# Optimization experiments

Hardware: AMD Instinct MI355X
Metric: run time of the kernel (lower is better)

Reference implementation:

```python
import jax, jax.numpy as jnp
import numpy as np


def _sum_matrix():
    # [69, 42] mask matrix reproducing compute_sums exactly (incl. bugs):
    # feature k = sum over cells where M[k] == 1, board flattened row-major (6x7).
    M = np.zeros((69, 42), dtype=np.float32)
    m = M.reshape(69, 6, 7)
    # 24 row window sums
    for row in range(6):
        for i in range(4):
            m[row * 4 + i, row, i:i + 4] = 1.0
    # 21 column window sums
    for col in range(7):
        for i in range(3):
            m[24 + col * 3 + i, i:i + 4, col] = 1.0
    # 12 'upward diag' sums: source sums the FULL 4x4 block of the row-flipped
    # board, i.e. original rows (2-off)..(5-off), cols col..col+3.
    for off in range(3):
        for col in range(4):
            m[45 + off * 4 + col, 2 - off:6 - off, col:col + 4] = 1.0
    # 12 'downward diag' sums: allocated but never written in source -> zeros.
    return jnp.asarray(M)


_M = _sum_matrix()  # [69, 42]


def setup_inputs() -> dict:
    key = jax.random.key(0)
    k1, k2, k3 = jax.random.split(key, 3)
    B = 524288
    game_state = jax.random.normal(k1, (B, 42), dtype=jnp.float32)
    W = jax.random.normal(k2, (7, 111), dtype=jnp.float32) * (1.0 / np.sqrt(111.0))
    b = jax.random.normal(k3, (7,), dtype=jnp.float32) * 0.01
    return {"game_state": game_state, "W": W, "b": b}


def reference(game_state, W, b):
    # sums: [B, 69] = all windowed sums as one GEMM against the mask matrix
    sums = game_state @ _M.T
    feats = jnp.concatenate([game_state, sums], axis=1)  # [B, 111]
    return feats @ W.T + b  # [B, 7]
```

## Files before the change

kernel.cpp:

```cpp
#include <hip/hip_runtime.h>


#define TILE_ROWS 128
#define ROW_PAD   43

__global__ __launch_bounds__(320)
void ddqn_weff(const float* __restrict__ W, float* __restrict__ weff) {
    int tid = threadIdx.x;
    if (tid >= 7 * 42) return;
    int j = tid / 42;
    int d = tid % 42;
    float acc = W[j * 111 + d];
    int r = d / 7, c = d % 7;
    const float* ws = W + j * 111 + 42;
    for (int i = 0; i < 4; ++i)
        if (c >= i && c <= i + 3) acc += ws[r * 4 + i];
    for (int i = 0; i < 3; ++i)
        if (r >= i && r <= i + 3) acc += ws[24 + c * 3 + i];
    for (int off = 0; off < 3; ++off)
        for (int col = 0; col < 4; ++col)
            if (r >= 2 - off && r <= 5 - off && c >= col && c <= col + 3)
                acc += ws[45 + off * 4 + col];
    weff[j * 42 + d] = acc;
}

__global__ __launch_bounds__(TILE_ROWS)
void ddqn_main(const float* __restrict__ gs,
               const float* __restrict__ weff,
               const float* __restrict__ b,
               float* __restrict__ out) {
    __shared__ float tile[TILE_ROWS * ROW_PAD];
    const int t = threadIdx.x;

    const float* src = gs + (size_t)blockIdx.x * (TILE_ROWS * 42);
    int row = t / 42;
    int col = t - row * 42;
    #pragma unroll
    for (int k = 0; k < 42; ++k) {
        tile[row * ROW_PAD + col] = src[k * TILE_ROWS + t];
        row += 3; col += 2;
        if (col >= 42) { col -= 42; row += 1; }
    }
    __syncthreads();

    float x[42];
    #pragma unroll
    for (int d = 0; d < 42; ++d) x[d] = tile[t * ROW_PAD + d];

    float acc[7];
    #pragma unroll
    for (int j = 0; j < 7; ++j) acc[j] = b[j];

    #pragma unroll
    for (int d = 0; d < 42; ++d) {
        #pragma unroll
        for (int j = 0; j < 7; ++j)
            acc[j] = fmaf(x[d], weff[j * 42 + d], acc[j]);
    }

    size_t gid = (size_t)blockIdx.x * TILE_ROWS + t;
    float* o = out + gid * 7;
    #pragma unroll
    for (int j = 0; j < 7; ++j) o[j] = acc[j];
}

extern "C" void kernel_launch(void* const* d_in, const int* in_sizes, int n_in,
                              void* d_out, int out_size, void* d_ws, size_t ws_size,
                              hipStream_t stream) {
    const float* gs = (const float*)d_in[0];
    const float* W  = (const float*)d_in[1];
    const float* b  = (const float*)d_in[2];
    float* out  = (float*)d_out;
    float* weff = (float*)d_ws;

    ddqn_weff<<<dim3(1), dim3(320), 0, stream>>>(W, weff);

    int B = in_sizes[0] / 42;
    ddqn_main<<<dim3(B / TILE_ROWS), dim3(TILE_ROWS), 0, stream>>>(gs, weff, b, out);
}
```

Baseline: 141.0 us.

## Use per-wave 64-row tiles with LDS-staged weights and wave barriers

Each block now holds four independent 64-row tiles, one per wavefront. The block-wide barrier after the tile load becomes a wave barrier, so waves proceed independently. The folded weights and bias are staged once per block in LDS, padded to 44 columns and read as float4 broadcasts instead of scalar global loads. This aims to cut per-row synchronisation and global weight traffic, at the cost of an extra block-level sync for the weight stage and somewhat more LDS per block.

```diff
diff --git a/kernel.cpp b/kernel.cpp
--- a/kernel.cpp
+++ b/kernel.cpp
@@ -1,8 +1,7 @@
 #include <hip/hip_runtime.h>
 
 
-#define TILE_ROWS 128
-#define ROW_PAD   43
+#define ROW_PAD 43
 
 __global__ __launch_bounds__(320)
 void ddqn_weff(const float* __restrict__ W, float* __restrict__ weff) {
@@ -24,42 +23,62 @@
     weff[j * 42 + d] = acc;
 }
 
-__global__ __launch_bounds__(TILE_ROWS)
+__global__ __launch_bounds__(256)
 void ddqn_main(const float* __restrict__ gs,
                const float* __restrict__ weff,
                const float* __restrict__ b,
                float* __restrict__ out) {
-    __shared__ float tile[TILE_ROWS * ROW_PAD];
+    __shared__ float wl[7 * 44 + 8];
+    __shared__ float tile[4][64 * ROW_PAD];
+
     const int t = threadIdx.x;
+    for (int i = t; i < 7 * 44; i += 256) {
+        int j = i / 44, d = i % 44;
+        wl[i] = (d < 42) ? weff[j * 42 + d] : 0.0f;
+    }
+    if (t < 7) wl[7 * 44 + t] = b[t];
+    __syncthreads();
 
-    const float* src = gs + (size_t)blockIdx.x * (TILE_ROWS * 42);
-    int row = t / 42;
-    int col = t - row * 42;
+    const int w = t >> 6;
+    const int l = t & 63;
+    float* tw = tile[w];
+
+    const size_t tileIdx = (size_t)blockIdx.x * 4 + w;
+    const float* src = gs + tileIdx * (64 * 42);
+
+    int row = l / 42;
+    int col = l - row * 42;
     #pragma unroll
     for (int k = 0; k < 42; ++k) {
-        tile[row * ROW_PAD + col] = src[k * TILE_ROWS + t];
-        row += 3; col += 2;
+        tw[row * ROW_PAD + col] = src[k * 64 + l];
+        row += 1; col += 22;
         if (col >= 42) { col -= 42; row += 1; }
     }
-    __syncthreads();
-
-    float x[42];
-    #pragma unroll
-    for (int d = 0; d < 42; ++d) x[d] = tile[t * ROW_PAD + d];
+    __builtin_amdgcn_wave_barrier();
 
     float acc[7];
     #pragma unroll
-    for (int j = 0; j < 7; ++j) acc[j] = b[j];
+    for (int j = 0; j < 7; ++j) acc[j] = wl[7 * 44 + j];
 
+    const float* xrow = tw + l * ROW_PAD;
+    const float4* wl4 = (const float4*)wl;
     #pragma unroll
-    for (int d = 0; d < 42; ++d) {
+    for (int dq = 0; dq < 44; dq += 4) {
+        float x0 = xrow[dq];
+        float x1 = xrow[dq + 1];
+        float x2 = (dq + 2 < 42) ? xrow[dq + 2] : 0.0f;
+        float x3 = (dq + 3 < 42) ? xrow[dq + 3] : 0.0f;
         #pragma unroll
-        for (int j = 0; j < 7; ++j)
-            acc[j] = fmaf(x[d], weff[j * 42 + d], acc[j]);
+        for (int j = 0; j < 7; ++j) {
+            const float4 wv = wl4[j * 11 + (dq >> 2)];
+            acc[j] = fmaf(x0, wv.x, acc[j]);
+            acc[j] = fmaf(x1, wv.y, acc[j]);
+            acc[j] = fmaf(x2, wv.z, acc[j]);
+            acc[j] = fmaf(x3, wv.w, acc[j]);
+        }
     }
 
-    size_t gid = (size_t)blockIdx.x * TILE_ROWS + t;
-    float* o = out + gid * 7;
+    float* o = out + (tileIdx * 64 + l) * 7;
     #pragma unroll
     for (int j = 0; j < 7; ++j) o[j] = acc[j];
 }
@@ -76,5 +95,6 @@
     ddqn_weff<<<dim3(1), dim3(320), 0, stream>>>(W, weff);
 
     int B = in_sizes[0] / 42;
-    ddqn_main<<<dim3(B / TILE_ROWS), dim3(TILE_ROWS), 0, stream>>>(gs, weff, b, out);
+    int tiles = B / 64;
+    ddqn_main<<<dim3(tiles / 4), dim3(256), 0, stream>>>(gs, weff, b, out);
 }
```

After: 143.2 us. Within noise of the previous version (+1.5%).
